# Optimization experiments

Hardware: AMD Instinct MI355X
Metric: run time of the kernel (lower is better)

## Reference

```python
import jax, jax.numpy as jnp
import numpy as np

EMBED_DIM = 256
NUM_CLASSES = 10


def setup_inputs() -> dict:
    key = jax.random.key(0)
    k1, k2, k3, k4 = jax.random.split(key, 4)
    x = jax.random.normal(k1, (64, 196, 768), dtype=jnp.float32)
    ag_w = jax.random.normal(k2, (EMBED_DIM, 768), dtype=jnp.float32)
    ag_b = jax.random.normal(k3, (EMBED_DIM,), dtype=jnp.float32)
    lm_w = jax.random.normal(k4, (EMBED_DIM * NUM_CLASSES, 768), dtype=jnp.float32)
    return {"x": x, "ag_w": ag_w, "ag_b": ag_b, "lm_w": lm_w}


def reference(x, ag_w, ag_b, lm_w):
    # x: (B, HW, D); ag_w: (E, D); ag_b: (E,); lm_w: (E*C, D)
    B, HW, D = x.shape
    E, C = EMBED_DIM, NUM_CLASSES
    # frozen arrangement generator -> binary sign pattern (B, HW, E)
    sign_patterns = (jnp.einsum('bhd,ed->bhe', x, ag_w) + ag_b > 0).astype(x.dtype)
    # linear map: (B, HW, E*C) -> (B, HW, E, C)
    z = jnp.einsum('bhd,pd->bhp', x, lm_w).reshape(B, HW, E, C)
    # masked reduction over HW and embed dims
    preds = jnp.einsum('bhp,bhpc->bc', sign_patterns, z) / HW
    return preds / E
```

## Files before the change

### kernel.cpp

```cpp
#include <hip/hip_runtime.h>

#define B_    64
#define HW_   196
#define HWP_  224
#define D_    768
#define E_    256
#define C_    10
#define MP_   (B_*HWP_)
#define K3K_  (E_*D_)
#define K3NB_ 256

typedef _Float16 f16x8 __attribute__((ext_vector_type(8)));
typedef _Float16 f16x4 __attribute__((ext_vector_type(4)));
typedef _Float16 f16x2 __attribute__((ext_vector_type(2)));
typedef float  f32x4  __attribute__((ext_vector_type(4)));

__device__ __forceinline__ void gld_lds16(const void* g, void* l) {
  __builtin_amdgcn_global_load_lds((const __attribute__((address_space(1))) void*)g,
                                   (__attribute__((address_space(3))) void*)l, 16, 0, 0);
}

__global__ __launch_bounds__(256) void k0_prep(const float* __restrict__ w,
                                               _Float16* __restrict__ w16) {
  size_t i4 = ((size_t)blockIdx.x * 256 + threadIdx.x) * 4;
  float4 v = *(const float4*)&w[i4];
  f16x4 h;
  h[0] = (_Float16)v.x; h[1] = (_Float16)v.y;
  h[2] = (_Float16)v.z; h[3] = (_Float16)v.w;
  *(f16x4*)&w16[i4] = h;
}

__global__ __launch_bounds__(256) void k1_signs(const float* __restrict__ x,
                                                const _Float16* __restrict__ w16,
                                                const float* __restrict__ bias,
                                                _Float16* __restrict__ st,
                                                _Float16* __restrict__ xf) {
  __shared__ __align__(16) char smem[59392];
  const int m0 = blockIdx.x * 64;
  const int tid = threadIdx.x;
  const int wave = tid >> 6, lane = tid & 63;
  const int wn = wave * 64;
  const int q = lane >> 4, l15 = lane & 15;
  const int swq = (q ^ ((l15 >> 1) & 3)) * 8;

  const int ar = tid >> 2, ac = (tid & 3) * 8;
  const int am = m0 + ar;
  const int ab = am / HWP_;
  const int ahp = am - ab * HWP_;
  const bool avalid = (ahp < HW_);
  const float* aptr = &x[((size_t)ab * HW_ + (avalid ? ahp : 0)) * D_ + ac];

  const int swB = ((tid & 3) ^ ((tid >> 3) & 3)) * 8;
  const size_t offB = (size_t)(tid >> 2) * D_ + swB;

  f32x4 acc[4][4] = {};
  float4 aX0, aX1, aY0, aY1;

#define K1_LOADA(r0, r1, kk) do { \
    r0 = *(const float4*)&aptr[(kk)]; \
    r1 = *(const float4*)&aptr[(kk) + 4]; \
  } while (0)

#define K1_CONV(bufA, r0, r1, kk) do { \
    _Float16* AW = (_Float16*)(smem + 49152 + (bufA) * 5120); \
    float va[8] = {r0.x, r0.y, r0.z, r0.w, r1.x, r1.y, r1.z, r1.w}; \
    f16x8 hh; \
    _Pragma("unroll") \
    for (int j = 0; j < 8; j++) { \
      float vj = avalid ? va[j] : 0.0f; \
      hh[j] = (_Float16)vj; \
    } \
    *(f16x8*)&AW[ar * 40 + ac] = hh; \
    *(f16x8*)&xf[(size_t)am * D_ + (kk) + ac] = hh; \
  } while (0)

#define K1_DMAB(buf3, kk) do { \
    char* bb = smem + (buf3) * 16384; \
    _Pragma("unroll") \
    for (int c = 0; c < 4; c++) { \
      gld_lds16(&w16[offB + (size_t)c * 64 * D_ + (kk)], bb + c * 4096 + wave * 1024); \
    } \
  } while (0)

#define K1_COMPUTE(buf3, bufA) do { \
    const _Float16* BL = (const _Float16*)(smem + (buf3) * 16384); \
    const _Float16* AL = (const _Float16*)(smem + 49152 + (bufA) * 5120); \
    f16x8 ah[4], bh[4]; \
    _Pragma("unroll") \
    for (int t = 0; t < 4; t++) { \
      ah[t] = *(const f16x8*)&AL[(t * 16 + l15) * 40 + q * 8]; \
      bh[t] = *(const f16x8*)&BL[(wn + t * 16 + l15) * 32 + swq]; \
    } \
    __builtin_amdgcn_s_setprio(1); \
    _Pragma("unroll") \
    for (int mt = 0; mt < 4; mt++) \
      _Pragma("unroll") \
      for (int nt = 0; nt < 4; nt++) \
        acc[mt][nt] = __builtin_amdgcn_mfma_f32_16x16x32_f16(ah[mt], bh[nt], acc[mt][nt], 0, 0, 0); \
    __builtin_amdgcn_s_setprio(0); \
  } while (0)

#define K1_BAR() do { \
    asm volatile("s_waitcnt lgkmcnt(0)" ::: "memory"); \
    __builtin_amdgcn_s_barrier(); \
    __builtin_amdgcn_sched_barrier(0); \
  } while (0)

  K1_DMAB(0, 0);
  __builtin_amdgcn_sched_barrier(0);
  K1_LOADA(aX0, aX1, 0);
  __builtin_amdgcn_sched_barrier(0);
  K1_DMAB(1, 32);
  __builtin_amdgcn_sched_barrier(0);
  K1_LOADA(aY0, aY1, 32);
  K1_CONV(0, aX0, aX1, 0);
  K1_BAR();

#pragma unroll
  for (int t = 0; t < 22; ++t) {
    K1_DMAB((t + 2) % 3, (t + 2) * 32);
    __builtin_amdgcn_sched_barrier(0);
    if ((t & 1) == 0) K1_LOADA(aX0, aX1, (t + 2) * 32);
    else              K1_LOADA(aY0, aY1, (t + 2) * 32);
    K1_COMPUTE(t % 3, t & 1);
    if ((t & 1) == 0) K1_CONV(1, aY0, aY1, (t + 1) * 32);
    else              K1_CONV(0, aX0, aX1, (t + 1) * 32);
    K1_BAR();
  }
  K1_COMPUTE(22 % 3, 0);
  K1_CONV(1, aY0, aY1, 23 * 32);
  K1_BAR();
  K1_COMPUTE(23 % 3, 1);
  K1_BAR();

#undef K1_LOADA
#undef K1_CONV
#undef K1_DMAB
#undef K1_COMPUTE
#undef K1_BAR

  _Float16* Sload = (_Float16*)smem;
#pragma unroll
  for (int mt = 0; mt < 4; mt++)
#pragma unroll
    for (int nt = 0; nt < 4; nt++) {
      int e = wn + nt * 16 + l15;
      float bv = bias[e];
      f16x4 o;
#pragma unroll
      for (int r = 0; r < 4; r++) {
        int m = m0 + mt * 16 + q * 4 + r;
        int b = m / HWP_;
        int hp = m - b * HWP_;
        float v = acc[mt][nt][r] + bv;
        o[r] = (hp < HW_ && v > 0.0f) ? (_Float16)1.0f : (_Float16)0.0f;
      }
      *(f16x4*)&Sload[e * 72 + mt * 16 + q * 4] = o;
    }
  __syncthreads();
#pragma unroll
  for (int it = 0; it < 16; it++) {
    int e = (tid >> 4) + it * 16;
    int m4 = (tid & 15) * 4;
    f16x4 v = *(const f16x4*)&Sload[e * 72 + m4];
    int mabs = m0 + m4;
    int b = mabs / HWP_;
    int hp = mabs - b * HWP_;
    *(f16x4*)&st[((size_t)b * E_ + e) * HWP_ + hp] = v;
  }
}

__global__ __launch_bounds__(256) void k2_g(const _Float16* __restrict__ st,
                                            const _Float16* __restrict__ xf,
                                            _Float16* __restrict__ g) {
  __shared__ __align__(16) _Float16 As[2][128 * 32];
  __shared__ __align__(16) _Float16 Bs[2][128 * 40];
  const int f = blockIdx.x;
  const int xcd = f & 7;
  const int s = f >> 3;
  const int b  = xcd + 8 * (s / 12);
  const int r12 = s % 12;
  const int eh = r12 / 6;
  const int d0 = (r12 % 6) * 128;
  const int tid = threadIdx.x;
  const int wave = tid >> 6, lane = tid & 63;
  const int WEl = (wave & 1) * 64;
  const int WD  = (wave >> 1) * 64;
  const int q = lane >> 4, l15 = lane & 15;
  const int ar = tid >> 2, ac = (tid & 3) * 8;
  const int ldA = wave * 512;
  const int dg = tid & 31, kp = tid >> 5;
  f32x4 acc[4][4] = {};

  const _Float16* gA = &st[((size_t)b * E_ + eh * 128 + ar) * HWP_ + ac];
  f16x4 h0, h1, h2, h3;

#define K2_STAGEA(buf, kk) do { \
    gld_lds16(gA + (kk),                      &As[buf][ldA]); \
    gld_lds16(gA + (size_t)64 * HWP_ + (kk),  &As[buf][2048 + ldA]); \
  } while (0)

#define K2_LOADB(kk) do { \
    const _Float16* bsrc = &xf[((size_t)b * HWP_ + (kk) + 4 * kp) * D_ + d0 + 4 * dg]; \
    h0 = *(const f16x4*)&bsrc[0]; \
    h1 = *(const f16x4*)&bsrc[D_]; \
    h2 = *(const f16x4*)&bsrc[2 * D_]; \
    h3 = *(const f16x4*)&bsrc[3 * D_]; \
  } while (0)

#define K2_WRITEB(buf) do { \
    _Pragma("unroll") \
    for (int j = 0; j < 4; j++) { \
      f16x4 o; \
      o[0] = h0[j]; o[1] = h1[j]; o[2] = h2[j]; o[3] = h3[j]; \
      *(f16x4*)&Bs[buf][(4 * dg + j) * 40 + 4 * kp] = o; \
    } \
  } while (0)

  K2_STAGEA(0, 0);
  K2_LOADB(0);
  K2_WRITEB(0);
  __syncthreads();

  int cur = 0;
  for (int k0 = 0; k0 < HWP_; k0 += 32) {
    const bool have = (k0 + 32 < HWP_);
    if (have) {
      K2_STAGEA(cur ^ 1, k0 + 32);
      K2_LOADB(k0 + 32);
    }
    f16x8 af[4], bfr[4];
#pragma unroll
    for (int t = 0; t < 4; t++) {
      af[t]  = *(const f16x8*)&As[cur][(WEl + t * 16 + l15) * 32 + q * 8];
      bfr[t] = *(const f16x8*)&Bs[cur][(WD + t * 16 + l15) * 40 + q * 8];
    }
#pragma unroll
    for (int mt = 0; mt < 4; mt++)
#pragma unroll
      for (int nt = 0; nt < 4; nt++)
        acc[mt][nt] = __builtin_amdgcn_mfma_f32_16x16x32_f16(af[mt], bfr[nt], acc[mt][nt], 0, 0, 0);
    if (have) K2_WRITEB(cur ^ 1);
    __syncthreads();
    cur ^= 1;
  }
#undef K2_STAGEA
#undef K2_LOADB
#undef K2_WRITEB

#pragma unroll
  for (int mt = 0; mt < 4; mt++)
#pragma unroll
    for (int nt = 0; nt < 4; nt++) {
      int d = d0 + WD + nt * 16 + l15;
#pragma unroll
      for (int r = 0; r < 4; r++) {
        int e = eh * 128 + WEl + mt * 16 + q * 4 + r;
        g[((size_t)b * E_ + e) * D_ + d] = (_Float16)acc[mt][nt][r];
      }
    }
}

__global__ __launch_bounds__(512) void k3_mfma(const _Float16* __restrict__ g,
                                               const float* __restrict__ lmw,
                                               float* __restrict__ part) {
  __shared__ float sp[B_ * C_];
  const int tid = threadIdx.x;
  const int wave = tid >> 6, lane = tid & 63;
  const int q = lane >> 4, l15 = lane & 15;
  const int e = blockIdx.x;
  f32x4 acc[4] = {};

  for (int i = tid; i < B_ * C_; i += 512) sp[i] = 0.0f;

#pragma unroll
  for (int ks = 0; ks < 3; ks++) {
    int d = wave * 96 + ks * 32 + q * 8;
    size_t k = (size_t)e * D_ + d;
    f16x8 bfrag;
    if (l15 < C_) {
      const float* bp = &lmw[((size_t)e * C_ + l15) * D_ + d];
      float4 b0 = *(const float4*)&bp[0];
      float4 b1 = *(const float4*)&bp[4];
      float bb[8] = {b0.x, b0.y, b0.z, b0.w, b1.x, b1.y, b1.z, b1.w};
#pragma unroll
      for (int j = 0; j < 8; j++) bfrag[j] = (_Float16)bb[j];
    } else {
#pragma unroll
      for (int j = 0; j < 8; j++) bfrag[j] = (_Float16)0.0f;
    }
#pragma unroll
    for (int mt = 0; mt < 4; mt++) {
      f16x8 afrag = *(const f16x8*)&g[(size_t)(mt * 16 + l15) * K3K_ + k];
      acc[mt] = __builtin_amdgcn_mfma_f32_16x16x32_f16(afrag, bfrag, acc[mt], 0, 0, 0);
    }
  }
  __syncthreads();
  if (l15 < C_) {
#pragma unroll
    for (int mt = 0; mt < 4; mt++)
#pragma unroll
      for (int r = 0; r < 4; r++) {
        int b = mt * 16 + q * 4 + r;
        atomicAdd(&sp[b * C_ + l15], acc[mt][r]);
      }
  }
  __syncthreads();
  for (int i = tid; i < B_ * C_; i += 512)
    part[(size_t)blockIdx.x * (B_ * C_) + i] = sp[i];
}

__global__ __launch_bounds__(256) void k4_reduce(const float* __restrict__ part,
                                                 float* __restrict__ out) {
  __shared__ float sp[256];
  const int b = blockIdx.x;
  const int tid = threadIdx.x;
  const int c = tid & 15, g16 = tid >> 4;
  float s = 0.0f;
  if (c < C_) {
#pragma unroll
    for (int j = 0; j < 16; j++)
      s += part[(size_t)(g16 + 16 * j) * (B_ * C_) + b * C_ + c];
  }
  sp[tid] = s;
  __syncthreads();
  if (tid < C_) {
    float t = 0.0f;
#pragma unroll
    for (int j = 0; j < 16; j++) t += sp[j * 16 + tid];
    out[b * C_ + tid] = t * (1.0f / (196.0f * 256.0f));
  }
}

extern "C" void kernel_launch(void* const* d_in, const int* in_sizes, int n_in,
                              void* d_out, int out_size, void* d_ws, size_t ws_size,
                              hipStream_t stream) {
  const float* x    = (const float*)d_in[0];
  const float* ag_w = (const float*)d_in[1];
  const float* ag_b = (const float*)d_in[2];
  const float* lm_w = (const float*)d_in[3];
  float* out = (float*)d_out;

  char* ws = (char*)d_ws;
  const size_t W_BYTES  = (size_t)E_ * D_ * 2;
  const size_t ST_BYTES = (size_t)B_ * E_ * HWP_ * 2;
  const size_t G_BYTES  = (size_t)B_ * E_ * D_ * 2;
  const size_t XF_BYTES = (size_t)MP_ * D_ * 2;
  _Float16* w16 = (_Float16*)(ws);
  _Float16* st  = (_Float16*)(ws + W_BYTES);
  _Float16* gb  = (_Float16*)(ws + W_BYTES + ST_BYTES);
  _Float16* xf  = (_Float16*)(ws + W_BYTES + ST_BYTES + G_BYTES);
  float*  part  = (float*)(ws + W_BYTES + ST_BYTES + G_BYTES + XF_BYTES);

  k0_prep<<<dim3((E_ * D_) / 4 / 256), dim3(256), 0, stream>>>(ag_w, w16);
  k1_signs<<<dim3(MP_ / 64), dim3(256), 0, stream>>>(x, w16, ag_b, st, xf);
  k2_g<<<dim3(12 * B_), dim3(256), 0, stream>>>(st, xf, gb);
  k3_mfma<<<dim3(K3NB_), dim3(512), 0, stream>>>(gb, lm_w, part);
  k4_reduce<<<dim3(B_), dim3(256), 0, stream>>>(part, out);
}
```

Baseline: 140.9 us.

## Move x fp16 conversion into prep kernel and DMA A tiles to LDS

Converts and pads x to fp16 inside the prep kernel alongside the weight conversion, instead of doing it in the GEMM main loop of the sign kernel. The sign kernel then loads both A and B tiles with direct global-to-LDS DMA into a triple buffer using swizzled layout, and waits on vmcnt so loads stay in flight across iterations. This removes register staging and conversion ALU from the GEMM loop. In exchange, the padded fp16 copy of x is written and then read back, which adds a full extra pass through memory.

```diff
diff --git a/kernel.cpp b/kernel.cpp
--- a/kernel.cpp
+++ b/kernel.cpp
@@ -12,7 +12,6 @@
 
 typedef _Float16 f16x8 __attribute__((ext_vector_type(8)));
 typedef _Float16 f16x4 __attribute__((ext_vector_type(4)));
-typedef _Float16 f16x2 __attribute__((ext_vector_type(2)));
 typedef float  f32x4  __attribute__((ext_vector_type(4)));
 
 __device__ __forceinline__ void gld_lds16(const void* g, void* l) {
@@ -20,22 +19,38 @@
                                    (__attribute__((address_space(3))) void*)l, 16, 0, 0);
 }
 
-__global__ __launch_bounds__(256) void k0_prep(const float* __restrict__ w,
+__global__ __launch_bounds__(256) void k0_prep(const float* __restrict__ x,
+                                               const float* __restrict__ w,
+                                               _Float16* __restrict__ xf,
                                                _Float16* __restrict__ w16) {
-  size_t i4 = ((size_t)blockIdx.x * 256 + threadIdx.x) * 4;
-  float4 v = *(const float4*)&w[i4];
-  f16x4 h;
-  h[0] = (_Float16)v.x; h[1] = (_Float16)v.y;
-  h[2] = (_Float16)v.z; h[3] = (_Float16)v.w;
-  *(f16x4*)&w16[i4] = h;
-}
-
-__global__ __launch_bounds__(256) void k1_signs(const float* __restrict__ x,
+  int bid = blockIdx.x;
+  if (bid < 192) {
+    size_t i4 = ((size_t)bid * 256 + threadIdx.x) * 4;
+    float4 v = *(const float4*)&w[i4];
+    f16x4 h;
+    h[0] = (_Float16)v.x; h[1] = (_Float16)v.y;
+    h[2] = (_Float16)v.z; h[3] = (_Float16)v.w;
+    *(f16x4*)&w16[i4] = h;
+  } else {
+    size_t i4 = ((size_t)(bid - 192) * 256 + threadIdx.x) * 4;
+    int d = (int)(i4 % D_);
+    size_t row = i4 / D_;
+    int hp = (int)(row % HWP_);
+    int b  = (int)(row / HWP_);
+    float4 v = make_float4(0.f, 0.f, 0.f, 0.f);
+    if (hp < HW_) v = *(const float4*)&x[((size_t)b * HW_ + hp) * D_ + d];
+    f16x4 h;
+    h[0] = (_Float16)v.x; h[1] = (_Float16)v.y;
+    h[2] = (_Float16)v.z; h[3] = (_Float16)v.w;
+    *(f16x4*)&xf[i4] = h;
+  }
+}
+
+__global__ __launch_bounds__(256) void k1_signs(const _Float16* __restrict__ xf,
                                                 const _Float16* __restrict__ w16,
                                                 const float* __restrict__ bias,
-                                                _Float16* __restrict__ st,
-                                                _Float16* __restrict__ xf) {
-  __shared__ __align__(16) char smem[59392];
+                                                _Float16* __restrict__ st) {
+  __shared__ __align__(16) char smem[61440];
   const int m0 = blockIdx.x * 64;
   const int tid = threadIdx.x;
   const int wave = tid >> 6, lane = tid & 63;
@@ -43,52 +58,27 @@
   const int q = lane >> 4, l15 = lane & 15;
   const int swq = (q ^ ((l15 >> 1) & 3)) * 8;
 
-  const int ar = tid >> 2, ac = (tid & 3) * 8;
-  const int am = m0 + ar;
-  const int ab = am / HWP_;
-  const int ahp = am - ab * HWP_;
-  const bool avalid = (ahp < HW_);
-  const float* aptr = &x[((size_t)ab * HW_ + (avalid ? ahp : 0)) * D_ + ac];
-
-  const int swB = ((tid & 3) ^ ((tid >> 3) & 3)) * 8;
-  const size_t offB = (size_t)(tid >> 2) * D_ + swB;
+  const int sw = ((tid & 3) ^ ((tid >> 3) & 3)) * 8;
+  const size_t offA = (size_t)(m0 + (tid >> 2)) * D_ + sw;
+  const size_t offB = (size_t)(tid >> 2) * D_ + sw;
 
   f32x4 acc[4][4] = {};
-  float4 aX0, aX1, aY0, aY1;
-
-#define K1_LOADA(r0, r1, kk) do { \
-    r0 = *(const float4*)&aptr[(kk)]; \
-    r1 = *(const float4*)&aptr[(kk) + 4]; \
-  } while (0)
-
-#define K1_CONV(bufA, r0, r1, kk) do { \
-    _Float16* AW = (_Float16*)(smem + 49152 + (bufA) * 5120); \
-    float va[8] = {r0.x, r0.y, r0.z, r0.w, r1.x, r1.y, r1.z, r1.w}; \
-    f16x8 hh; \
-    _Pragma("unroll") \
-    for (int j = 0; j < 8; j++) { \
-      float vj = avalid ? va[j] : 0.0f; \
-      hh[j] = (_Float16)vj; \
-    } \
-    *(f16x8*)&AW[ar * 40 + ac] = hh; \
-    *(f16x8*)&xf[(size_t)am * D_ + (kk) + ac] = hh; \
-  } while (0)
-
-#define K1_DMAB(buf3, kk) do { \
+
+#define K1_DMA(buf3, kk) do { \
     char* bb = smem + (buf3) * 16384; \
     _Pragma("unroll") \
-    for (int c = 0; c < 4; c++) { \
+    for (int c = 0; c < 4; c++) \
       gld_lds16(&w16[offB + (size_t)c * 64 * D_ + (kk)], bb + c * 4096 + wave * 1024); \
-    } \
-  } while (0)
-
-#define K1_COMPUTE(buf3, bufA) do { \
+    gld_lds16(&xf[offA + (kk)], smem + 49152 + (buf3) * 4096 + wave * 1024); \
+  } while (0)
+
+#define K1_COMPUTE(buf3) do { \
     const _Float16* BL = (const _Float16*)(smem + (buf3) * 16384); \
-    const _Float16* AL = (const _Float16*)(smem + 49152 + (bufA) * 5120); \
+    const _Float16* AL = (const _Float16*)(smem + 49152 + (buf3) * 4096); \
     f16x8 ah[4], bh[4]; \
     _Pragma("unroll") \
     for (int t = 0; t < 4; t++) { \
-      ah[t] = *(const f16x8*)&AL[(t * 16 + l15) * 40 + q * 8]; \
+      ah[t] = *(const f16x8*)&AL[(t * 16 + l15) * 32 + swq]; \
       bh[t] = *(const f16x8*)&BL[(wn + t * 16 + l15) * 32 + swq]; \
     } \
     __builtin_amdgcn_s_setprio(1); \
@@ -100,44 +90,24 @@
     __builtin_amdgcn_s_setprio(0); \
   } while (0)
 
-#define K1_BAR() do { \
-    asm volatile("s_waitcnt lgkmcnt(0)" ::: "memory"); \
-    __builtin_amdgcn_s_barrier(); \
-    __builtin_amdgcn_sched_barrier(0); \
-  } while (0)
-
-  K1_DMAB(0, 0);
+  K1_DMA(0, 0);
+  K1_DMA(1, 32);
+  asm volatile("s_waitcnt vmcnt(5)" ::: "memory");
+  __builtin_amdgcn_s_barrier();
   __builtin_amdgcn_sched_barrier(0);
-  K1_LOADA(aX0, aX1, 0);
-  __builtin_amdgcn_sched_barrier(0);
-  K1_DMAB(1, 32);
-  __builtin_amdgcn_sched_barrier(0);
-  K1_LOADA(aY0, aY1, 32);
-  K1_CONV(0, aX0, aX1, 0);
-  K1_BAR();
-
-#pragma unroll
-  for (int t = 0; t < 22; ++t) {
-    K1_DMAB((t + 2) % 3, (t + 2) * 32);
+
+#pragma unroll
+  for (int t = 0; t < 24; ++t) {
+    if (t + 2 < 24) K1_DMA((t + 2) % 3, (t + 2) * 32);
     __builtin_amdgcn_sched_barrier(0);
-    if ((t & 1) == 0) K1_LOADA(aX0, aX1, (t + 2) * 32);
-    else              K1_LOADA(aY0, aY1, (t + 2) * 32);
-    K1_COMPUTE(t % 3, t & 1);
-    if ((t & 1) == 0) K1_CONV(1, aY0, aY1, (t + 1) * 32);
-    else              K1_CONV(0, aX0, aX1, (t + 1) * 32);
-    K1_BAR();
-  }
-  K1_COMPUTE(22 % 3, 0);
-  K1_CONV(1, aY0, aY1, 23 * 32);
-  K1_BAR();
-  K1_COMPUTE(23 % 3, 1);
-  K1_BAR();
-
-#undef K1_LOADA
-#undef K1_CONV
-#undef K1_DMAB
+    K1_COMPUTE(t % 3);
+    if (t + 2 < 24) asm volatile("s_waitcnt vmcnt(5) lgkmcnt(0)" ::: "memory");
+    else            asm volatile("s_waitcnt vmcnt(0) lgkmcnt(0)" ::: "memory");
+    __builtin_amdgcn_s_barrier();
+    __builtin_amdgcn_sched_barrier(0);
+  }
+#undef K1_DMA
 #undef K1_COMPUTE
-#undef K1_BAR
 
   _Float16* Sload = (_Float16*)smem;
 #pragma unroll
@@ -352,8 +322,8 @@
   _Float16* xf  = (_Float16*)(ws + W_BYTES + ST_BYTES + G_BYTES);
   float*  part  = (float*)(ws + W_BYTES + ST_BYTES + G_BYTES + XF_BYTES);
 
-  k0_prep<<<dim3((E_ * D_) / 4 / 256), dim3(256), 0, stream>>>(ag_w, w16);
-  k1_signs<<<dim3(MP_ / 64), dim3(256), 0, stream>>>(x, w16, ag_b, st, xf);
+  k0_prep<<<dim3(192 + (MP_ * D_) / 4 / 256), dim3(256), 0, stream>>>(x, ag_w, xf, w16);
+  k1_signs<<<dim3(MP_ / 64), dim3(256), 0, stream>>>(xf, w16, ag_b, st);
   k2_g<<<dim3(12 * B_), dim3(256), 0, stream>>>(st, xf, gb);
   k3_mfma<<<dim3(K3NB_), dim3(512), 0, stream>>>(gb, lm_w, part);
   k4_reduce<<<dim3(B_), dim3(256), 0, stream>>>(part, out);
```

Measured after the change: 131.8 us. -6.5%, faster.
